# Optimization experiments

Measured on AMD Instinct MI355X. Metric: run time of the kernel, lower is better.

Reference implementation:

```python
import jax, jax.numpy as jnp
import numpy as np

W1 = W2 = W3 = 7  # window size


def _rel_pos_indices(w1, w2, w3):
    # Static relative-position index table, matching the torch buffer.
    g = np.stack(np.meshgrid(np.arange(w1), np.arange(w2), np.arange(w3), indexing='ij'))
    g = g.reshape(3, -1).T                      # (N, 3), N = w1*w2*w3
    rel = g[:, None, :] - g[None, :, :]         # (N, N, 3)
    rel[..., 0] += w1 - 1
    rel[..., 1] += w2 - 1
    rel[..., 2] += w3 - 1
    strides = np.array([(2 * w2 - 1) * (2 * w3 - 1), 2 * w3 - 1, 1])
    return jnp.asarray((rel * strides).sum(-1), dtype=jnp.int32)  # (N, N)


def setup_inputs() -> dict:
    key = jax.random.key(0)
    k1, k2, k3, k4 = jax.random.split(key, 4)
    dim, heads = 256, 8
    x = jax.random.normal(k1, (2, 4, 4, 4, W1, W2, W3, dim), dtype=jnp.float32)
    w_qkv = jax.random.normal(k2, (dim, 3 * dim), dtype=jnp.float32) * (dim ** -0.5)
    w_out = jax.random.normal(k3, (dim, dim), dtype=jnp.float32) * (dim ** -0.5)
    n_rel = (2 * W1 - 1) * (2 * W2 - 1) * (2 * W3 - 1)  # 2197
    rel_bias_table = jax.random.normal(k4, (n_rel, heads), dtype=jnp.float32) * 0.02
    return {"x": x, "w_qkv": w_qkv, "w_out": w_out, "rel_bias_table": rel_bias_table}


def reference(x, w_qkv, w_out, rel_bias_table):
    b, gx, gy, gz, w1, w2, w3, d = x.shape
    heads = rel_bias_table.shape[1]
    dh = d // heads
    scale = dh ** -0.5
    n = w1 * w2 * w3
    B = b * gx * gy * gz

    xf = x.reshape(B, n, d)
    qkv = xf @ w_qkv                             # (B, n, 3d)
    q, k, v = jnp.split(qkv, 3, axis=-1)

    def to_heads(t):
        return t.reshape(B, n, heads, dh).transpose(0, 2, 1, 3)  # (B, h, n, dh)

    q, k, v = to_heads(q), to_heads(k), to_heads(v)

    rel_idx = _rel_pos_indices(w1, w2, w3)                       # (n, n)
    bias = rel_bias_table[rel_idx].transpose(2, 0, 1)            # (h, n, n)

    logits = jnp.einsum('bhnd,bhmd->bhnm', q, k) * scale + bias[None]
    attn = jax.nn.softmax(logits, axis=-1)
    ctx = jnp.einsum('bhnm,bhmd->bhnd', attn, v)                 # (B, h, n, dh)

    out = ctx.transpose(0, 2, 1, 3).reshape(B, n, d) @ w_out     # (B, n, d)
    return out.reshape(b, gx, gy, gz, w1, w2, w3, d)
```

## Files before the change

kernel.cpp:

```cpp
#include <hip/hip_runtime.h>
#include <math.h>

using f16   = _Float16;
using f16x4 = __attribute__((ext_vector_type(4))) _Float16;
using f16x8 = __attribute__((ext_vector_type(8))) _Float16;
using f32x4 = __attribute__((ext_vector_type(4))) float;

#define NW    343
#define NWP   352
#define VTP   356
#define HEADS 8
#define MTOT  43904
#define LOG2E 1.4426950408889634f
#define QSC   (0.17677669529663687f * 1.4426950408889634f)

typedef const __attribute__((address_space(1))) unsigned int* gp1_t;
typedef __attribute__((address_space(3))) unsigned int* lp3_t;
__device__ __forceinline__ void gload_lds16(const void* g, void* l) {
    __builtin_amdgcn_global_load_lds((gp1_t)g, (lp3_t)l, 16, 0, 0);
}

__global__ void cvt_x(const float* __restrict__ x, f16* __restrict__ xb) {
    int id = blockIdx.x * 256 + threadIdx.x;
    float4 v = *(const float4*)(x + id * 4);
    f16x4 o = { (f16)v.x, (f16)v.y, (f16)v.z, (f16)v.w };
    *(f16x4*)(xb + id * 4) = o;
}

__global__ void cvt_wT(const float* __restrict__ W, f16* __restrict__ WT,
                       int N, int scaleN, float sc) {
    int id = blockIdx.x * 256 + threadIdx.x;
    int n = id >> 8, k = id & 255;
    float v = W[k * N + n];
    if (n < scaleN) v *= sc;
    WT[n * 256 + k] = (f16)v;
}

__global__ void bias_k(const float* __restrict__ tab, float* __restrict__ bp) {
    int id = blockIdx.x * 256 + threadIdx.x;
    int h = id / (NWP * NWP);
    int rem = id - h * NWP * NWP;
    int i = rem / NWP, j = rem - (rem / NWP) * NWP;
    float v;
    if (j >= NW) v = -1e30f;
    else if (i >= NW) v = 0.f;
    else {
        int a1 = i / 49, a2 = (i / 7) % 7, a3 = i % 7;
        int b1 = j / 49, b2 = (j / 7) % 7, b3 = j % 7;
        int idx = (a1 - b1 + 6) * 169 + (a2 - b2 + 6) * 13 + (a3 - b3 + 6);
        v = tab[idx * 8 + h] * LOG2E;
    }
    bp[id] = v;
}

template<bool OUT_F32>
__launch_bounds__(256)
__global__ void gemm_k(const f16* __restrict__ A, const f16* __restrict__ Bt,
                       void* __restrict__ Cp, int N) {
    __shared__ f16 As[128 * 32];
    __shared__ f16 Bs[128 * 32];
    const int m0 = blockIdx.x * 128;
    const int n0 = blockIdx.y * 128;
    const int t = threadIdx.x;
    const int wave = t >> 6, lane = t & 63;
    const int q = lane >> 4, c = lane & 15;
    const int wm = (wave >> 1) * 64, wn = (wave & 1) * 64;
    const int r0 = t >> 2;
    const int c8 = (t & 3) * 8;

    f32x4 acc[4][4] = {};
#pragma unroll
    for (int ks = 0; ks < 256; ks += 32) {
        gload_lds16(&A[(size_t)(m0 + r0) * 256 + ks + c8],        &As[r0 * 32 + c8]);
        gload_lds16(&A[(size_t)(m0 + r0 + 64) * 256 + ks + c8],   &As[(r0 + 64) * 32 + c8]);
        gload_lds16(&Bt[(size_t)(n0 + r0) * 256 + ks + c8],       &Bs[r0 * 32 + c8]);
        gload_lds16(&Bt[(size_t)(n0 + r0 + 64) * 256 + ks + c8],  &Bs[(r0 + 64) * 32 + c8]);
        __syncthreads();
        f16x8 af[4], bf[4];
#pragma unroll
        for (int a = 0; a < 4; a++) af[a] = *(const f16x8*)&As[(wm + a * 16 + c) * 32 + q * 8];
#pragma unroll
        for (int b = 0; b < 4; b++) bf[b] = *(const f16x8*)&Bs[(wn + b * 16 + c) * 32 + q * 8];
#pragma unroll
        for (int a = 0; a < 4; a++)
#pragma unroll
            for (int b = 0; b < 4; b++)
                acc[a][b] = __builtin_amdgcn_mfma_f32_16x16x32_f16(af[a], bf[b], acc[a][b], 0, 0, 0);
        __syncthreads();
    }
#pragma unroll
    for (int a = 0; a < 4; a++)
#pragma unroll
        for (int b = 0; b < 4; b++) {
            int row0 = m0 + wm + a * 16 + q * 4;
            int col = n0 + wn + b * 16 + c;
#pragma unroll
            for (int r = 0; r < 4; r++) {
                float v = acc[a][b][r];
                if (OUT_F32) ((float*)Cp)[(size_t)(row0 + r) * N + col] = v;
                else         ((f16*)Cp)[(size_t)(row0 + r) * N + col] = (f16)v;
            }
        }
}

__launch_bounds__(512)
__global__ void attn_k(const f16* __restrict__ qkv, const float* __restrict__ biasP,
                       f16* __restrict__ ctx) {
    const int w = blockIdx.x >> 3;
    const int h = blockIdx.x & 7;
    __shared__ f16 Ks[NWP * 32];
    __shared__ f16 Vt[32 * VTP];
    const int t = threadIdx.x;
    const size_t base = (size_t)(w * NW) * 768;

    for (int u = t; u < NWP * 4; u += 512) {
        int row = u >> 2, un = u & 3;
        uint4 val;
        if (row < NW) val = *(const uint4*)&qkv[base + (size_t)row * 768 + 256 + h * 32 + un * 8];
        else { val.x = val.y = val.z = val.w = 0u; }
        *(uint4*)&Ks[row * 32 + un * 8] = val;
    }
    for (int u = t; u < NWP * 4; u += 512) {
        int row = u >> 2, un = u & 3;
        if (row < NW) {
            uint4 val = *(const uint4*)&qkv[base + (size_t)row * 768 + 512 + h * 32 + un * 8];
            const f16* pv = (const f16*)&val;
#pragma unroll
            for (int e = 0; e < 8; e++) Vt[(un * 8 + e) * VTP + row] = pv[e];
        } else {
#pragma unroll
            for (int e = 0; e < 8; e++) Vt[(un * 8 + e) * VTP + row] = (f16)0.f;
        }
    }
    __syncthreads();

    const int wave = t >> 6, lane = t & 63;
    const int q = lane >> 4, c = lane & 15;
    const float* biasH = biasP + (size_t)h * NWP * NWP;

    for (int qt = wave; qt < NWP / 16; qt += 8) {
        const int iq = qt * 16 + c;
        const int iqc = iq < NW ? iq : NW - 1;
        f16x8 qf = *(const f16x8*)&qkv[base + (size_t)iqc * 768 + h * 32 + q * 8];
        const float* brow = biasH + (size_t)iq * NWP;

        f32x4 o0 = {0.f, 0.f, 0.f, 0.f}, o1 = {0.f, 0.f, 0.f, 0.f};
        float lsum = 0.f;
#pragma unroll
        for (int jt = 0; jt < NWP / 16; jt++) {
            const int jb = jt * 16;
            f16x8 kf = *(const f16x8*)&Ks[(jb + c) * 32 + q * 8];
            f32x4 z = {0.f, 0.f, 0.f, 0.f};
            f32x4 s = __builtin_amdgcn_mfma_f32_16x16x32_f16(kf, qf, z, 0, 0, 0);
            f32x4 b4 = *(const f32x4*)&brow[jb + q * 4];
            float p0 = __builtin_amdgcn_exp2f(s[0] + b4[0]);
            float p1 = __builtin_amdgcn_exp2f(s[1] + b4[1]);
            float p2 = __builtin_amdgcn_exp2f(s[2] + b4[2]);
            float p3 = __builtin_amdgcn_exp2f(s[3] + b4[3]);
            lsum += (p0 + p1) + (p2 + p3);
            f16x4 pf = { (f16)p0, (f16)p1, (f16)p2, (f16)p3 };
            f16x4 v0 = *(const f16x4*)&Vt[c * VTP + jb + q * 4];
            f16x4 v1 = *(const f16x4*)&Vt[(16 + c) * VTP + jb + q * 4];
            o0 = __builtin_amdgcn_mfma_f32_16x16x16f16(v0, pf, o0, 0, 0, 0);
            o1 = __builtin_amdgcn_mfma_f32_16x16x16f16(v1, pf, o1, 0, 0, 0);
        }
        lsum += __shfl_xor(lsum, 16);
        lsum += __shfl_xor(lsum, 32);

        if (iq < NW) {
            float inv = 1.f / lsum;
            size_t ob = (size_t)(w * NW + iq) * 256 + h * 32;
            f16x4 s0 = { (f16)(o0[0] * inv), (f16)(o0[1] * inv),
                         (f16)(o0[2] * inv), (f16)(o0[3] * inv) };
            f16x4 s1 = { (f16)(o1[0] * inv), (f16)(o1[1] * inv),
                         (f16)(o1[2] * inv), (f16)(o1[3] * inv) };
            *(f16x4*)&ctx[ob + q * 4] = s0;
            *(f16x4*)&ctx[ob + 16 + q * 4] = s1;
        }
    }
}

extern "C" void kernel_launch(void* const* d_in, const int* in_sizes, int n_in,
                              void* d_out, int out_size, void* d_ws, size_t ws_size,
                              hipStream_t stream) {
    const float* x    = (const float*)d_in[0];
    const float* wqkv = (const float*)d_in[1];
    const float* wout = (const float*)d_in[2];
    const float* tab  = (const float*)d_in[3];

    char* ws = (char*)d_ws;
    size_t off = 0;
    f16*   xb     = (f16*)(ws + off);   off += (size_t)MTOT * 256 * 2;
    f16*   wqkvT  = (f16*)(ws + off);   off += (size_t)768 * 256 * 2;
    f16*   woutT  = (f16*)(ws + off);   off += (size_t)256 * 256 * 2;
    float* biasP  = (float*)(ws + off); off += (size_t)8 * NWP * NWP * 4;
    f16*   qkvb   = (f16*)(ws + off);   off += (size_t)MTOT * 768 * 2;
    f16*   ctxb   = (f16*)(ws + off);   off += (size_t)MTOT * 256 * 2;
    if (ws_size < off) return;

    cvt_x <<<MTOT * 256 / 1024, 256, 0, stream>>>(x, xb);
    cvt_wT<<<768, 256, 0, stream>>>(wqkv, wqkvT, 768, 256, QSC);
    cvt_wT<<<256, 256, 0, stream>>>(wout, woutT, 256, 0, 1.f);
    bias_k<<<8 * NWP * NWP / 256, 256, 0, stream>>>(tab, biasP);
    gemm_k<false><<<dim3(MTOT / 128, 768 / 128), 256, 0, stream>>>(xb, wqkvT, qkvb, 768);
    attn_k<<<128 * HEADS, 512, 0, stream>>>(qkvb, biasP, ctxb);
    gemm_k<true><<<dim3(MTOT / 128, 256 / 128), 256, 0, stream>>>(ctxb, woutT, d_out, 256);
}
```

Baseline: 234.5 us.

## Process two query tiles per wave in attention with 256-thread blocks

The attention kernel now uses 4 waves per block, and each wave handles two 16-row query tiles at once. Each K and V fragment read from LDS is reused for both tiles, giving two independent MFMA/exp chains to interleave. The bias is folded into the MFMA accumulator input instead of being added after the QK product. Smaller blocks with launch bounds of 3 may change occupancy, and higher register use plus uneven tile counts per wave are the risks.

After: 229.2 us. 2.3% less time.

```diff
diff --git a/kernel.cpp b/kernel.cpp
--- a/kernel.cpp
+++ b/kernel.cpp
@@ -103,7 +103,85 @@
         }
 }
 
-__launch_bounds__(512)
+template<bool HASB>
+__device__ __forceinline__ void attn_tiles(
+    const f16* __restrict__ qkv, const float* __restrict__ biasH,
+    f16* __restrict__ ctx, const f16* Ks, const f16* Vt,
+    size_t base, int w, int h, int q, int c, int ta, int tb)
+{
+    const int iqa = ta * 16 + c;
+    const int iqb = tb * 16 + c;
+    const int iqac = iqa < NW ? iqa : NW - 1;
+    const int iqbc = iqb < NW ? iqb : NW - 1;
+    f16x8 qfa = *(const f16x8*)&qkv[base + (size_t)iqac * 768 + h * 32 + q * 8];
+    f16x8 qfb{};
+    if constexpr (HASB) qfb = *(const f16x8*)&qkv[base + (size_t)iqbc * 768 + h * 32 + q * 8];
+    const float* browA = biasH + (size_t)iqa * NWP;
+    const float* browB = biasH + (size_t)iqb * NWP;
+
+    f32x4 o0a = {0.f,0.f,0.f,0.f}, o1a = {0.f,0.f,0.f,0.f};
+    f32x4 o0b = {0.f,0.f,0.f,0.f}, o1b = {0.f,0.f,0.f,0.f};
+    float lsa = 0.f, lsb = 0.f;
+#pragma unroll
+    for (int jt = 0; jt < NWP / 16; jt++) {
+        const int jb = jt * 16;
+        f16x8 kf = *(const f16x8*)&Ks[(jb + c) * 32 + q * 8];
+        f16x4 v0 = *(const f16x4*)&Vt[c * VTP + jb + q * 4];
+        f16x4 v1 = *(const f16x4*)&Vt[(16 + c) * VTP + jb + q * 4];
+
+        f32x4 ba = *(const f32x4*)&browA[jb + q * 4];
+        f32x4 sa = __builtin_amdgcn_mfma_f32_16x16x32_f16(kf, qfa, ba, 0, 0, 0);
+        float pa0 = __builtin_amdgcn_exp2f(sa[0]);
+        float pa1 = __builtin_amdgcn_exp2f(sa[1]);
+        float pa2 = __builtin_amdgcn_exp2f(sa[2]);
+        float pa3 = __builtin_amdgcn_exp2f(sa[3]);
+        lsa += (pa0 + pa1) + (pa2 + pa3);
+        f16x4 pfa = { (f16)pa0, (f16)pa1, (f16)pa2, (f16)pa3 };
+        o0a = __builtin_amdgcn_mfma_f32_16x16x16f16(v0, pfa, o0a, 0, 0, 0);
+        o1a = __builtin_amdgcn_mfma_f32_16x16x16f16(v1, pfa, o1a, 0, 0, 0);
+
+        if constexpr (HASB) {
+            f32x4 bb = *(const f32x4*)&browB[jb + q * 4];
+            f32x4 sb = __builtin_amdgcn_mfma_f32_16x16x32_f16(kf, qfb, bb, 0, 0, 0);
+            float pb0 = __builtin_amdgcn_exp2f(sb[0]);
+            float pb1 = __builtin_amdgcn_exp2f(sb[1]);
+            float pb2 = __builtin_amdgcn_exp2f(sb[2]);
+            float pb3 = __builtin_amdgcn_exp2f(sb[3]);
+            lsb += (pb0 + pb1) + (pb2 + pb3);
+            f16x4 pfb = { (f16)pb0, (f16)pb1, (f16)pb2, (f16)pb3 };
+            o0b = __builtin_amdgcn_mfma_f32_16x16x16f16(v0, pfb, o0b, 0, 0, 0);
+            o1b = __builtin_amdgcn_mfma_f32_16x16x16f16(v1, pfb, o1b, 0, 0, 0);
+        }
+    }
+    lsa += __shfl_xor(lsa, 16);
+    lsa += __shfl_xor(lsa, 32);
+    if (iqa < NW) {
+        float inv = 1.f / lsa;
+        size_t ob = (size_t)(w * NW + iqa) * 256 + h * 32;
+        f16x4 s0 = { (f16)(o0a[0] * inv), (f16)(o0a[1] * inv),
+                     (f16)(o0a[2] * inv), (f16)(o0a[3] * inv) };
+        f16x4 s1 = { (f16)(o1a[0] * inv), (f16)(o1a[1] * inv),
+                     (f16)(o1a[2] * inv), (f16)(o1a[3] * inv) };
+        *(f16x4*)&ctx[ob + q * 4] = s0;
+        *(f16x4*)&ctx[ob + 16 + q * 4] = s1;
+    }
+    if constexpr (HASB) {
+        lsb += __shfl_xor(lsb, 16);
+        lsb += __shfl_xor(lsb, 32);
+        if (iqb < NW) {
+            float inv = 1.f / lsb;
+            size_t ob = (size_t)(w * NW + iqb) * 256 + h * 32;
+            f16x4 s0 = { (f16)(o0b[0] * inv), (f16)(o0b[1] * inv),
+                         (f16)(o0b[2] * inv), (f16)(o0b[3] * inv) };
+            f16x4 s1 = { (f16)(o1b[0] * inv), (f16)(o1b[1] * inv),
+                         (f16)(o1b[2] * inv), (f16)(o1b[3] * inv) };
+            *(f16x4*)&ctx[ob + q * 4] = s0;
+            *(f16x4*)&ctx[ob + 16 + q * 4] = s1;
+        }
+    }
+}
+
+__launch_bounds__(256, 3)
 __global__ void attn_k(const f16* __restrict__ qkv, const float* __restrict__ biasP,
                        f16* __restrict__ ctx) {
     const int w = blockIdx.x >> 3;
@@ -113,14 +191,14 @@
     const int t = threadIdx.x;
     const size_t base = (size_t)(w * NW) * 768;
 
-    for (int u = t; u < NWP * 4; u += 512) {
+    for (int u = t; u < NWP * 4; u += 256) {
         int row = u >> 2, un = u & 3;
         uint4 val;
         if (row < NW) val = *(const uint4*)&qkv[base + (size_t)row * 768 + 256 + h * 32 + un * 8];
         else { val.x = val.y = val.z = val.w = 0u; }
         *(uint4*)&Ks[row * 32 + un * 8] = val;
     }
-    for (int u = t; u < NWP * 4; u += 512) {
+    for (int u = t; u < NWP * 4; u += 256) {
         int row = u >> 2, un = u & 3;
         if (row < NW) {
             uint4 val = *(const uint4*)&qkv[base + (size_t)row * 768 + 512 + h * 32 + un * 8];
@@ -138,45 +216,13 @@
     const int q = lane >> 4, c = lane & 15;
     const float* biasH = biasP + (size_t)h * NWP * NWP;
 
-    for (int qt = wave; qt < NWP / 16; qt += 8) {
-        const int iq = qt * 16 + c;
-        const int iqc = iq < NW ? iq : NW - 1;
-        f16x8 qf = *(const f16x8*)&qkv[base + (size_t)iqc * 768 + h * 32 + q * 8];
-        const float* brow = biasH + (size_t)iq * NWP;
-
-        f32x4 o0 = {0.f, 0.f, 0.f, 0.f}, o1 = {0.f, 0.f, 0.f, 0.f};
-        float lsum = 0.f;
-#pragma unroll
-        for (int jt = 0; jt < NWP / 16; jt++) {
-            const int jb = jt * 16;
-            f16x8 kf = *(const f16x8*)&Ks[(jb + c) * 32 + q * 8];
-            f32x4 z = {0.f, 0.f, 0.f, 0.f};
-            f32x4 s = __builtin_amdgcn_mfma_f32_16x16x32_f16(kf, qf, z, 0, 0, 0);
-            f32x4 b4 = *(const f32x4*)&brow[jb + q * 4];
-            float p0 = __builtin_amdgcn_exp2f(s[0] + b4[0]);
-            float p1 = __builtin_amdgcn_exp2f(s[1] + b4[1]);
-            float p2 = __builtin_amdgcn_exp2f(s[2] + b4[2]);
-            float p3 = __builtin_amdgcn_exp2f(s[3] + b4[3]);
-            lsum += (p0 + p1) + (p2 + p3);
-            f16x4 pf = { (f16)p0, (f16)p1, (f16)p2, (f16)p3 };
-            f16x4 v0 = *(const f16x4*)&Vt[c * VTP + jb + q * 4];
-            f16x4 v1 = *(const f16x4*)&Vt[(16 + c) * VTP + jb + q * 4];
-            o0 = __builtin_amdgcn_mfma_f32_16x16x16f16(v0, pf, o0, 0, 0, 0);
-            o1 = __builtin_amdgcn_mfma_f32_16x16x16f16(v1, pf, o1, 0, 0, 0);
-        }
-        lsum += __shfl_xor(lsum, 16);
-        lsum += __shfl_xor(lsum, 32);
-
-        if (iq < NW) {
-            float inv = 1.f / lsum;
-            size_t ob = (size_t)(w * NW + iq) * 256 + h * 32;
-            f16x4 s0 = { (f16)(o0[0] * inv), (f16)(o0[1] * inv),
-                         (f16)(o0[2] * inv), (f16)(o0[3] * inv) };
-            f16x4 s1 = { (f16)(o1[0] * inv), (f16)(o1[1] * inv),
-                         (f16)(o1[2] * inv), (f16)(o1[3] * inv) };
-            *(f16x4*)&ctx[ob + q * 4] = s0;
-            *(f16x4*)&ctx[ob + 16 + q * 4] = s1;
-        }
+#pragma unroll
+    for (int pass = 0; pass < 3; pass++) {
+        int p = wave + 4 * pass;
+        if (p < 10)
+            attn_tiles<true >(qkv, biasH, ctx, Ks, Vt, base, w, h, q, c, 2 * p, 2 * p + 1);
+        else
+            attn_tiles<false>(qkv, biasH, ctx, Ks, Vt, base, w, h, q, c, p + 10, p + 10);
     }
 }
 
@@ -203,6 +249,6 @@
     cvt_wT<<<256, 256, 0, stream>>>(wout, woutT, 256, 0, 1.f);
     bias_k<<<8 * NWP * NWP / 256, 256, 0, stream>>>(tab, biasP);
     gemm_k<false><<<dim3(MTOT / 128, 768 / 128), 256, 0, stream>>>(xb, wqkvT, qkvb, 768);
-    attn_k<<<128 * HEADS, 512, 0, stream>>>(qkvb, biasP, ctxb);
+    attn_k<<<128 * HEADS, 256, 0, stream>>>(qkvb, biasP, ctxb);
     gemm_k<true><<<dim3(MTOT / 128, 256 / 128), 256, 0, stream>>>(ctxb, woutT, d_out, 256);
 }
```

## Process multiple query tiles per wave in attention to reuse K/V fragments

Applied to the files above, without the earlier changes.

The attention kernel drops from 512 to 256 threads per block. Each of the 4 waves now handles 5 or 6 query tiles at once, so every K and V fragment read from LDS is reused across those tiles. The bias is also fed in as the MFMA accumulator initializer, which removes separate adds. The cost is many more registers per wave and fewer waves per block, which could hurt latency hiding, and the launch bounds are set to 3 blocks per CU.

Result: no change. 230.7 us (-1.6%).

```diff
diff --git a/kernel.cpp b/kernel.cpp
--- a/kernel.cpp
+++ b/kernel.cpp
@@ -103,7 +103,69 @@
         }
 }
 
-__launch_bounds__(512)
+template<int NT>
+__device__ __forceinline__ void attn_tiles(
+    const f16* __restrict__ qkv, const float* __restrict__ biasH,
+    f16* __restrict__ ctx, const f16* Ks, const f16* Vt,
+    size_t base, int w, int h, int q, int c, int t0)
+{
+    f16x8 qf[NT];
+    f32x4 o0[NT], o1[NT];
+    float ls[NT];
+#pragma unroll
+    for (int i = 0; i < NT; i++) {
+        int iq = (t0 + i) * 16 + c;
+        int iqc = iq < NW ? iq : NW - 1;
+        qf[i] = *(const f16x8*)&qkv[base + (size_t)iqc * 768 + h * 32 + q * 8];
+        o0[i] = (f32x4){0.f, 0.f, 0.f, 0.f};
+        o1[i] = (f32x4){0.f, 0.f, 0.f, 0.f};
+        ls[i] = 0.f;
+    }
+    const float* brow0 = biasH + (size_t)(t0 * 16 + c) * NWP + q * 4;
+
+#pragma unroll 2
+    for (int jt = 0; jt < NWP / 16; jt++) {
+        const int jb = jt * 16;
+        f16x8 kf = *(const f16x8*)&Ks[(jb + c) * 32 + q * 8];
+        f16x4 v0 = *(const f16x4*)&Vt[c * VTP + jb + q * 4];
+        f16x4 v1 = *(const f16x4*)&Vt[(16 + c) * VTP + jb + q * 4];
+        f32x4 b[NT];
+#pragma unroll
+        for (int i = 0; i < NT; i++)
+            b[i] = *(const f32x4*)&brow0[i * 16 * NWP + jb];
+#pragma unroll
+        for (int i = 0; i < NT; i++) {
+            f32x4 s = __builtin_amdgcn_mfma_f32_16x16x32_f16(kf, qf[i], b[i], 0, 0, 0);
+            float p0 = __builtin_amdgcn_exp2f(s[0]);
+            float p1 = __builtin_amdgcn_exp2f(s[1]);
+            float p2 = __builtin_amdgcn_exp2f(s[2]);
+            float p3 = __builtin_amdgcn_exp2f(s[3]);
+            ls[i] += (p0 + p1) + (p2 + p3);
+            f16x4 pf = { (f16)p0, (f16)p1, (f16)p2, (f16)p3 };
+            o0[i] = __builtin_amdgcn_mfma_f32_16x16x16f16(v0, pf, o0[i], 0, 0, 0);
+            o1[i] = __builtin_amdgcn_mfma_f32_16x16x16f16(v1, pf, o1[i], 0, 0, 0);
+        }
+    }
+#pragma unroll
+    for (int i = 0; i < NT; i++) {
+        float l = ls[i];
+        l += __shfl_xor(l, 16);
+        l += __shfl_xor(l, 32);
+        int iq = (t0 + i) * 16 + c;
+        if (iq < NW) {
+            float inv = 1.f / l;
+            size_t ob = (size_t)(w * NW + iq) * 256 + h * 32;
+            f16x4 s0 = { (f16)(o0[i][0] * inv), (f16)(o0[i][1] * inv),
+                         (f16)(o0[i][2] * inv), (f16)(o0[i][3] * inv) };
+            f16x4 s1 = { (f16)(o1[i][0] * inv), (f16)(o1[i][1] * inv),
+                         (f16)(o1[i][2] * inv), (f16)(o1[i][3] * inv) };
+            *(f16x4*)&ctx[ob + q * 4] = s0;
+            *(f16x4*)&ctx[ob + 16 + q * 4] = s1;
+        }
+    }
+}
+
+__launch_bounds__(256, 3)
 __global__ void attn_k(const f16* __restrict__ qkv, const float* __restrict__ biasP,
                        f16* __restrict__ ctx) {
     const int w = blockIdx.x >> 3;
@@ -113,14 +175,14 @@
     const int t = threadIdx.x;
     const size_t base = (size_t)(w * NW) * 768;
 
-    for (int u = t; u < NWP * 4; u += 512) {
+    for (int u = t; u < NWP * 4; u += 256) {
         int row = u >> 2, un = u & 3;
         uint4 val;
         if (row < NW) val = *(const uint4*)&qkv[base + (size_t)row * 768 + 256 + h * 32 + un * 8];
         else { val.x = val.y = val.z = val.w = 0u; }
         *(uint4*)&Ks[row * 32 + un * 8] = val;
     }
-    for (int u = t; u < NWP * 4; u += 512) {
+    for (int u = t; u < NWP * 4; u += 256) {
         int row = u >> 2, un = u & 3;
         if (row < NW) {
             uint4 val = *(const uint4*)&qkv[base + (size_t)row * 768 + 512 + h * 32 + un * 8];
@@ -138,46 +200,10 @@
     const int q = lane >> 4, c = lane & 15;
     const float* biasH = biasP + (size_t)h * NWP * NWP;
 
-    for (int qt = wave; qt < NWP / 16; qt += 8) {
-        const int iq = qt * 16 + c;
-        const int iqc = iq < NW ? iq : NW - 1;
-        f16x8 qf = *(const f16x8*)&qkv[base + (size_t)iqc * 768 + h * 32 + q * 8];
-        const float* brow = biasH + (size_t)iq * NWP;
-
-        f32x4 o0 = {0.f, 0.f, 0.f, 0.f}, o1 = {0.f, 0.f, 0.f, 0.f};
-        float lsum = 0.f;
-#pragma unroll
-        for (int jt = 0; jt < NWP / 16; jt++) {
-            const int jb = jt * 16;
-            f16x8 kf = *(const f16x8*)&Ks[(jb + c) * 32 + q * 8];
-            f32x4 z = {0.f, 0.f, 0.f, 0.f};
-            f32x4 s = __builtin_amdgcn_mfma_f32_16x16x32_f16(kf, qf, z, 0, 0, 0);
-            f32x4 b4 = *(const f32x4*)&brow[jb + q * 4];
-            float p0 = __builtin_amdgcn_exp2f(s[0] + b4[0]);
-            float p1 = __builtin_amdgcn_exp2f(s[1] + b4[1]);
-            float p2 = __builtin_amdgcn_exp2f(s[2] + b4[2]);
-            float p3 = __builtin_amdgcn_exp2f(s[3] + b4[3]);
-            lsum += (p0 + p1) + (p2 + p3);
-            f16x4 pf = { (f16)p0, (f16)p1, (f16)p2, (f16)p3 };
-            f16x4 v0 = *(const f16x4*)&Vt[c * VTP + jb + q * 4];
-            f16x4 v1 = *(const f16x4*)&Vt[(16 + c) * VTP + jb + q * 4];
-            o0 = __builtin_amdgcn_mfma_f32_16x16x16f16(v0, pf, o0, 0, 0, 0);
-            o1 = __builtin_amdgcn_mfma_f32_16x16x16f16(v1, pf, o1, 0, 0, 0);
-        }
-        lsum += __shfl_xor(lsum, 16);
-        lsum += __shfl_xor(lsum, 32);
-
-        if (iq < NW) {
-            float inv = 1.f / lsum;
-            size_t ob = (size_t)(w * NW + iq) * 256 + h * 32;
-            f16x4 s0 = { (f16)(o0[0] * inv), (f16)(o0[1] * inv),
-                         (f16)(o0[2] * inv), (f16)(o0[3] * inv) };
-            f16x4 s1 = { (f16)(o1[0] * inv), (f16)(o1[1] * inv),
-                         (f16)(o1[2] * inv), (f16)(o1[3] * inv) };
-            *(f16x4*)&ctx[ob + q * 4] = s0;
-            *(f16x4*)&ctx[ob + 16 + q * 4] = s1;
-        }
-    }
+    if      (wave == 0) attn_tiles<6>(qkv, biasH, ctx, Ks, Vt, base, w, h, q, c, 0);
+    else if (wave == 1) attn_tiles<6>(qkv, biasH, ctx, Ks, Vt, base, w, h, q, c, 6);
+    else if (wave == 2) attn_tiles<5>(qkv, biasH, ctx, Ks, Vt, base, w, h, q, c, 12);
+    else                attn_tiles<5>(qkv, biasH, ctx, Ks, Vt, base, w, h, q, c, 17);
 }
 
 extern "C" void kernel_launch(void* const* d_in, const int* in_sizes, int n_in,
@@ -203,6 +229,6 @@
     cvt_wT<<<256, 256, 0, stream>>>(wout, woutT, 256, 0, 1.f);
     bias_k<<<8 * NWP * NWP / 256, 256, 0, stream>>>(tab, biasP);
     gemm_k<false><<<dim3(MTOT / 128, 768 / 128), 256, 0, stream>>>(xb, wqkvT, qkvb, 768);
-    attn_k<<<128 * HEADS, 512, 0, stream>>>(qkvb, biasP, ctxb);
+    attn_k<<<128 * HEADS, 256, 0, stream>>>(qkvb, biasP, ctxb);
     gemm_k<true><<<dim3(MTOT / 128, 256 / 128), 256, 0, stream>>>(ctxb, woutT, d_out, 256);
 }
```
